# Performance work log

Measured on AMD Instinct MI355X. Metric: run time of the kernel, lower is better.

## Reference

```python
import jax, jax.numpy as jnp
import numpy as np

BN_EPS = 1e-3
SLOPE = 0.1
K = 100
CLUSTER_TEMP = 5.0


def setup_inputs() -> dict:
    key = jax.random.key(0)
    ks = jax.random.split(key, 5)
    N, Cin, Cout = 8192, 1, 64
    d = 49 * Cout  # (28/4)^2 * out_channels
    return {
        "x": jax.random.normal(ks[0], (N, Cin, 28, 28), jnp.float32),
        "conv1_w": jax.random.normal(ks[1], (128, Cin, 5, 5), jnp.float32) * 0.05,
        "conv1_b": jnp.zeros((128,), jnp.float32),
        "bn1_gamma": jnp.ones((128,), jnp.float32),
        "bn1_beta": jnp.zeros((128,), jnp.float32),
        "bn1_mean": jnp.zeros((128,), jnp.float32),
        "bn1_var": jnp.ones((128,), jnp.float32),
        "conv2_w": jax.random.normal(ks[2], (Cout, 128, 5, 5), jnp.float32) * 0.02,
        "conv2_b": jnp.zeros((Cout,), jnp.float32),
        "bn2_gamma": jnp.ones((Cout,), jnp.float32),
        "bn2_beta": jnp.zeros((Cout,), jnp.float32),
        "bn2_mean": jnp.zeros((Cout,), jnp.float32),
        "bn2_var": jnp.ones((Cout,), jnp.float32),
        "init_mu": jax.random.uniform(ks[3], (K, d), jnp.float32),
        "num_iter": 10,
    }


def _conv_bn_lrelu(x, w, b, gamma, beta, mean, var):
    # Conv2d(k=5, s=2, p=2) -> BatchNorm (eval/running stats) -> LeakyReLU(0.1)
    h = jax.lax.conv_general_dilated(
        x, w, window_strides=(2, 2), padding=[(2, 2), (2, 2)],
        dimension_numbers=("NCHW", "OIHW", "NCHW"))
    h = h + b[None, :, None, None]
    inv = gamma * jax.lax.rsqrt(var + BN_EPS)
    h = h * inv[None, :, None, None] + (beta - mean * inv)[None, :, None, None]
    return jnp.where(h >= 0, h, SLOPE * h)


def _cluster(data, mu, num_iter):
    # Row L2-normalize (equivalent to diag(1/||row||) @ data)
    data = data / jnp.linalg.norm(data, axis=1, keepdims=True)  # [n, d]
    for _ in range(num_iter):
        dist = data @ mu.T                                 # [n, K]
        r = jax.nn.softmax(CLUSTER_TEMP * dist, axis=1)    # [n, K]
        cluster_r = r.sum(axis=0)                          # [K]
        cluster_mean = r.T @ data                          # [K, d]
        mu = cluster_mean / cluster_r[:, None]
    dist = data @ mu.T
    r = jax.nn.softmax(CLUSTER_TEMP * dist, axis=1)
    return mu, r, dist


def reference(x, conv1_w, conv1_b, bn1_gamma, bn1_beta, bn1_mean, bn1_var,
              conv2_w, conv2_b, bn2_gamma, bn2_beta, bn2_mean, bn2_var,
              init_mu, num_iter):
    h = _conv_bn_lrelu(x, conv1_w, conv1_b, bn1_gamma, bn1_beta, bn1_mean, bn1_var)
    h = _conv_bn_lrelu(h, conv2_w, conv2_b, bn2_gamma, bn2_beta, bn2_mean, bn2_var)
    embeds = h.reshape(h.shape[0], -1)                     # [N, 49*Cout]
    mu_init, _, _ = _cluster(embeds, init_mu, int(num_iter))
    mu, r, dist = _cluster(embeds, jax.lax.stop_gradient(mu_init), 1)
    return mu, r, dist
```

## Files before the change

kernel.cpp:

```cpp
#include <hip/hip_runtime.h>
#include <hip/hip_bf16.h>
#include <math.h>

#define BN_EPS 1e-3f
#define SLOPE  0.1f
#define TEMP   5.0f
#define DDIM   3136

typedef __attribute__((ext_vector_type(8))) short bf16x8;
typedef __attribute__((ext_vector_type(4))) float f32x4;

static __device__ __forceinline__ short f2b(float f) {
  __hip_bfloat16 h = __float2bfloat16(f);
  return *reinterpret_cast<short*>(&h);
}

#define W2B_OFF   0u
#define W1B_OFF   102400u
#define DB_OFF    204800u
#define DB_SZ     (8192u*3136u/2u)
#define DT_OFF    (DB_OFF + DB_SZ)
#define DT_SZ     (8192u*3136u/2u)
#define MUB_OFF   (DT_OFF + DT_SZ)
#define MUB_SZ    (112u*3136u/2u)
#define MUF_OFF   (MUB_OFF + MUB_SZ)
#define MUF_SZ    (100u*3136u)
#define CMS_OFF   (MUF_OFF + MUF_SZ)
#define CMS_SZ    (16u*3136u*112u/2u)
#define RT_OFF    (CMS_OFF + CMS_SZ)
#define RT_SZ     (112u*8192u/2u)
#define CR_OFF    (RT_OFF + RT_SZ)

__global__ __launch_bounds__(256) void k_w2b(const float* __restrict__ w2,
                                             __hip_bfloat16* __restrict__ w2b) {
  int idx = blockIdx.x * 256 + threadIdx.x;
  if (idx >= 204800) return;
  int ci   = idx & 31;
  int lr   = (idx >> 5) & 15;
  int rest = idx >> 9;
  int kk   = rest % 100;
  int oct  = rest / 100;
  int oc   = oct * 16 + lr;
  int tap  = kk >> 2;
  int c    = ((kk & 3) << 5) + ci;
  w2b[idx] = __float2bfloat16(w2[(oc * 128 + c) * 25 + tap]);
}

__global__ __launch_bounds__(256) void k_w1b(const float* __restrict__ w1,
                                             __hip_bfloat16* __restrict__ w1b) {
  int idx = blockIdx.x * 256 + threadIdx.x;
  if (idx >= 4096) return;
  int k   = idx & 31;
  int lr  = (idx >> 5) & 15;
  int oct = idx >> 9;
  int oc  = oct * 16 + lr;
  float v = (k < 25) ? w1[oc * 25 + k] : 0.f;
  w1b[idx] = __float2bfloat16(v);
}

__global__ __launch_bounds__(256) void k_conv(
    const float* __restrict__ x,
    const __hip_bfloat16* __restrict__ w1bh, const float* __restrict__ b1,
    const float* __restrict__ g1,  const float* __restrict__ be1,
    const float* __restrict__ mn1, const float* __restrict__ vr1,
    const __hip_bfloat16* __restrict__ w2bh, const float* __restrict__ b2,
    const float* __restrict__ g2,  const float* __restrict__ be2,
    const float* __restrict__ mn2, const float* __restrict__ vr2,
    __hip_bfloat16* __restrict__ db) {
  __shared__ float xs[1024];
  __shared__ float bn2s[128];
  __shared__ float bn1a[128], bn1b[128];
  __shared__ float nrm[4];
  __shared__ __align__(16) __hip_bfloat16 h1s[197 * 128];

  const int t    = threadIdx.x;
  const int img  = blockIdx.x;
  const int lane = t & 63;
  const int wv   = t >> 6;
  const int lr   = lane & 15;
  const int kg   = lane >> 4;
  const short* w2b = (const short*)w2bh;
  const short* w1b = (const short*)w1bh;

  for (int i = t; i < 1024; i += 256) xs[i] = 0.f;
  if (t < 64) {
    float a2 = g2[t] * rsqrtf(vr2[t] + BN_EPS);
    bn2s[t]      = a2;
    bn2s[64 + t] = b2[t] * a2 + be2[t] - mn2[t] * a2;
    ((unsigned*)(h1s + 196 * 128))[t] = 0u;
  }
  if (t < 128) {
    float a1 = g1[t] * rsqrtf(vr1[t] + BN_EPS);
    bn1a[t] = a1;
    bn1b[t] = b1[t] * a1 + be1[t] - mn1[t] * a1;
  }
  __syncthreads();
  const float* xi = x + (size_t)img * 784;
  for (int i = t; i < 784; i += 256) {
    int yy = i / 28, xx = i % 28;
    xs[(yy + 2) * 32 + (xx + 2)] = xi[i];
  }
  __syncthreads();

  {
    bf16x8 a0 = *(const bf16x8*)(w1b + (2 * wv) * 512 + lr * 32 + kg * 8);
    bf16x8 a1 = *(const bf16x8*)(w1b + (2 * wv + 1) * 512 + lr * 32 + kg * 8);
    for (int pt = 0; pt < 13; ++pt) {
      const int px  = pt * 16 + lr;
      const int pxc = (px < 196) ? px : 195;
      const int oy  = pxc / 14, ox = pxc - 14 * (pxc / 14);
      const float* xb = xs + (2 * oy) * 32 + 2 * ox;
      short bs[8];
#pragma unroll
      for (int j = 0; j < 8; ++j) {
        int k   = kg * 8 + j;
        int tap = (k < 25) ? k : 0;
        int kh  = tap / 5, kw = tap - 5 * (tap / 5);
        bs[j] = f2b(xb[kh * 32 + kw]);
      }
      bf16x8 b;
#pragma unroll
      for (int j = 0; j < 8; ++j) b[j] = bs[j];
      f32x4 c0 = {0.f, 0.f, 0.f, 0.f}, c1 = {0.f, 0.f, 0.f, 0.f};
      c0 = __builtin_amdgcn_mfma_f32_16x16x32_bf16(a0, b, c0, 0, 0, 0);
      c1 = __builtin_amdgcn_mfma_f32_16x16x32_bf16(a1, b, c1, 0, 0, 0);
      if (px < 196) {
        const int swz = (px & 7) << 4;
        unsigned w0lo, w0hi, w1lo, w1hi;
        {
          float v[4], u[4];
#pragma unroll
          for (int r = 0; r < 4; ++r) {
            int oc = wv * 32 + kg * 4 + r;
            float h = c0[r] * bn1a[oc] + bn1b[oc];
            v[r] = (h >= 0.f) ? h : SLOPE * h;
            int oc2 = oc + 16;
            float h2 = c1[r] * bn1a[oc2] + bn1b[oc2];
            u[r] = (h2 >= 0.f) ? h2 : SLOPE * h2;
          }
          w0lo = (unsigned)(unsigned short)f2b(v[0]) |
                 ((unsigned)(unsigned short)f2b(v[1]) << 16);
          w0hi = (unsigned)(unsigned short)f2b(v[2]) |
                 ((unsigned)(unsigned short)f2b(v[3]) << 16);
          w1lo = (unsigned)(unsigned short)f2b(u[0]) |
                 ((unsigned)(unsigned short)f2b(u[1]) << 16);
          w1hi = (unsigned)(unsigned short)f2b(u[2]) |
                 ((unsigned)(unsigned short)f2b(u[3]) << 16);
        }
        char* base = (char*)h1s + px * 256;
        const int o0 = ((wv * 32 + kg * 4) * 2) ^ swz;
        const int o1 = ((wv * 32 + 16 + kg * 4) * 2) ^ swz;
        *(uint2*)(base + o0) = make_uint2(w0lo, w0hi);
        *(uint2*)(base + o1) = make_uint2(w1lo, w1hi);
      }
    }
  }
  __syncthreads();

  const int woff  = lr * 32 + kg * 8;
  const int kgoff = kg << 4;
  int pxA[4], oyA[4], oxA[4];
#pragma unroll
  for (int pt = 0; pt < 4; ++pt) {
    int p = pt * 16 + lr;
    pxA[pt] = p;
    oyA[pt] = p / 7;
    oxA[pt] = p - 7 * oyA[pt];
  }

  f32x4 acc[4][4];
#pragma unroll
  for (int oct = 0; oct < 4; ++oct)
#pragma unroll
    for (int pt = 0; pt < 4; ++pt) acc[oct][pt] = (f32x4){0.f, 0.f, 0.f, 0.f};

  const int s0 = 25 * wv, s1e = s0 + 25;
  int curtap = -1;
  int rowB[4], rowS[4];

  auto loadk = [&](int kk, bf16x8* areg, bf16x8* breg) {
    int tap = kk >> 2;
    if (tap != curtap) {
      curtap = tap;
      int kh = tap / 5, kw = tap - 5 * (tap / 5);
#pragma unroll
      for (int pt = 0; pt < 4; ++pt) {
        int iy = 2 * oyA[pt] - 2 + kh;
        int ix = 2 * oxA[pt] - 2 + kw;
        bool val = (pxA[pt] < 49) & ((unsigned)iy < 14u) & ((unsigned)ix < 14u);
        int ip = val ? iy * 14 + ix : 196;
        rowB[pt] = ip * 256;
        rowS[pt] = (ip & 7) << 4;
      }
    }
    int c01 = (kk & 3) << 6;
#pragma unroll
    for (int oct = 0; oct < 4; ++oct)
      areg[oct] = *(const bf16x8*)(w2b + ((oct * 100 + kk) << 9) + woff);
#pragma unroll
    for (int pt = 0; pt < 4; ++pt)
      breg[pt] = *(const bf16x8*)((const char*)h1s + rowB[pt] +
                                  ((c01 | kgoff) ^ rowS[pt]));
  };

  bf16x8 a[4], b[4], an[4], bn_[4];
  loadk(s0, a, b);
  for (int kk = s0; kk < s1e; ++kk) {
    if (kk + 1 < s1e) loadk(kk + 1, an, bn_);
#pragma unroll
    for (int oct = 0; oct < 4; ++oct)
#pragma unroll
      for (int pt = 0; pt < 4; ++pt)
        acc[oct][pt] = __builtin_amdgcn_mfma_f32_16x16x32_bf16(a[oct], b[pt],
                                                               acc[oct][pt], 0, 0, 0);
#pragma unroll
    for (int q = 0; q < 4; ++q) { a[q] = an[q]; b[q] = bn_[q]; }
  }
  __syncthreads();

  float* red = (float*)h1s;
  if (wv != 0) {
#pragma unroll
    for (int oct = 0; oct < 4; ++oct)
#pragma unroll
      for (int pt = 0; pt < 4; ++pt)
#pragma unroll
        for (int r = 0; r < 4; ++r)
          red[(wv - 1) * 4096 + ((oct * 4 + pt) * 4 + r) * 64 + lane] =
              acc[oct][pt][r];
  }
  __syncthreads();
  if (wv == 0) {
#pragma unroll
    for (int oct = 0; oct < 4; ++oct)
#pragma unroll
      for (int pt = 0; pt < 4; ++pt)
#pragma unroll
        for (int r = 0; r < 4; ++r) {
          const int i = (oct * 4 + pt) * 4 + r;
          float v = acc[oct][pt][r] + red[i * 64 + lane] +
                    red[4096 + i * 64 + lane] + red[8192 + i * 64 + lane];
          red[i * 64 + lane] = v;
        }
  }
  __syncthreads();

  float outv[16];
  float ss = 0.f;
#pragma unroll
  for (int pt = 0; pt < 4; ++pt) {
#pragma unroll
    for (int r = 0; r < 4; ++r) {
      const int i = ((wv * 4 + pt) * 4 + r);
      float v = red[i * 64 + lane];
      const int oc = wv * 16 + kg * 4 + r;
      v = v * bn2s[oc] + bn2s[64 + oc];
      v = (v >= 0.f) ? v : SLOPE * v;
      outv[pt * 4 + r] = v;
      if (pxA[pt] < 49) ss += v * v;
    }
  }
#pragma unroll
  for (int m = 1; m < 64; m <<= 1) ss += __shfl_xor(ss, m, 64);
  if (lane == 0) nrm[wv] = ss;
  __syncthreads();
  const float invn = rsqrtf(nrm[0] + nrm[1] + nrm[2] + nrm[3]);
  __hip_bfloat16* dro = db + (size_t)img * DDIM;
#pragma unroll
  for (int pt = 0; pt < 4; ++pt) {
    if (pxA[pt] < 49) {
#pragma unroll
      for (int r = 0; r < 4; ++r) {
        const int oc = wv * 16 + kg * 4 + r;
        dro[oc * 49 + pxA[pt]] = __float2bfloat16(outv[pt * 4 + r] * invn);
      }
    }
  }
}

__global__ __launch_bounds__(256) void k_tr(const __hip_bfloat16* __restrict__ dbh,
                                            __hip_bfloat16* __restrict__ dTh) {
  __shared__ short tile[64][72];
  const int t   = threadIdx.x;
  const int i   = t >> 2;
  const int seg = t & 3;
  const size_t img0 = (size_t)blockIdx.x * 64;
  const size_t d0   = (size_t)blockIdx.y * 64;
  const short* src = (const short*)dbh + (img0 + i) * DDIM + d0 + seg * 16;
  bf16x8 v0 = *(const bf16x8*)src;
  bf16x8 v1 = *(const bf16x8*)(src + 8);
  *(bf16x8*)&tile[i][seg * 16]     = v0;
  *(bf16x8*)&tile[i][seg * 16 + 8] = v1;
  __syncthreads();
  short tmp[16];
#pragma unroll
  for (int k = 0; k < 16; ++k) tmp[k] = tile[seg * 16 + k][i];
  short* dst = (short*)dTh + (d0 + i) * 8192 + img0 + seg * 16;
  *(bf16x8*)dst       = *(bf16x8*)tmp;
  *(bf16x8*)(dst + 8) = *((bf16x8*)tmp + 1);
}

__global__ __launch_bounds__(256) void k_muinit(const float* __restrict__ mu0,
                                                __hip_bfloat16* __restrict__ mub) {
  int idx = blockIdx.x * 256 + threadIdx.x;
  if (idx >= 112 * DDIM) return;
  int j = idx / DDIM, d = idx - j * DDIM;
  float v = (j < 100) ? mu0[j * DDIM + d] : 0.f;
  mub[idx] = __float2bfloat16(v);
}

__global__ __launch_bounds__(512) void k_dsm(
    const __hip_bfloat16* __restrict__ data,
    const __hip_bfloat16* __restrict__ mu,
    __hip_bfloat16* __restrict__ rT,
    float* __restrict__ cr,
    float* __restrict__ outr,
    float* __restrict__ outd,
    int final_flag) {
  __shared__ float red[7][64][29];
  const int t    = threadIdx.x;
  const int lane = t & 63;
  const int wv   = t >> 6;
  const int rowbase = blockIdx.x * 16;
  const int s0 = (98 * wv) >> 3;
  const int s1 = (98 * (wv + 1)) >> 3;
  const int lr = lane & 15;
  const int kg = lane >> 4;

  const __hip_bfloat16* arow = data + (size_t)(rowbase + lr) * DDIM + kg * 8;
  const __hip_bfloat16* brow = mu + (size_t)lr * DDIM + kg * 8;

  f32x4 acc[7];
#pragma unroll
  for (int i = 0; i < 7; ++i) acc[i] = (f32x4){0.f, 0.f, 0.f, 0.f};

  bf16x8 a, b[7], an, bn_[7];
  {
    const int k0 = s0 * 32;
    a = *(const bf16x8*)(arow + k0);
#pragma unroll
    for (int tl = 0; tl < 7; ++tl)
      b[tl] = *(const bf16x8*)(brow + (size_t)tl * 16 * DDIM + k0);
  }
  for (int s = s0; s < s1; ++s) {
    if (s + 1 < s1) {
      const int k1 = (s + 1) * 32;
      an = *(const bf16x8*)(arow + k1);
#pragma unroll
      for (int tl = 0; tl < 7; ++tl)
        bn_[tl] = *(const bf16x8*)(brow + (size_t)tl * 16 * DDIM + k1);
    }
#pragma unroll
    for (int tl = 0; tl < 7; ++tl)
      acc[tl] = __builtin_amdgcn_mfma_f32_16x16x32_bf16(a, b[tl], acc[tl], 0, 0, 0);
    a = an;
#pragma unroll
    for (int tl = 0; tl < 7; ++tl) b[tl] = bn_[tl];
  }

  if (wv != 0) {
#pragma unroll
    for (int tl = 0; tl < 7; ++tl)
#pragma unroll
      for (int r = 0; r < 4; ++r) red[wv - 1][lane][tl * 4 + r] = acc[tl][r];
  }
  __syncthreads();
  if (wv != 0) return;

#pragma unroll
  for (int tl = 0; tl < 7; ++tl)
#pragma unroll
    for (int r = 0; r < 4; ++r) {
      float v = acc[tl][r];
#pragma unroll
      for (int bk = 0; bk < 7; ++bk) v += red[bk][lane][tl * 4 + r];
      acc[tl][r] = v;
    }

  if (final_flag) {
#pragma unroll
    for (int tl = 0; tl < 7; ++tl) {
      const int col = tl * 16 + lr;
      if (col < 100) {
#pragma unroll
        for (int r = 0; r < 4; ++r)
          outd[(size_t)(rowbase + kg * 4 + r) * 100 + col] = acc[tl][r];
      }
    }
  }

#pragma unroll
  for (int r = 0; r < 4; ++r) {
    float m = -1e30f;
#pragma unroll
    for (int tl = 0; tl < 7; ++tl) {
      const bool valid = (tl < 6) || (lr < 4);
      m = fmaxf(m, valid ? acc[tl][r] : -1e30f);
    }
    m = fmaxf(m, __shfl_xor(m, 1, 64));
    m = fmaxf(m, __shfl_xor(m, 2, 64));
    m = fmaxf(m, __shfl_xor(m, 4, 64));
    m = fmaxf(m, __shfl_xor(m, 8, 64));
    float s = 0.f;
    float e[7];
#pragma unroll
    for (int tl = 0; tl < 7; ++tl) {
      const bool valid = (tl < 6) || (lr < 4);
      e[tl] = valid ? __expf(TEMP * (acc[tl][r] - m)) : 0.f;
      s += e[tl];
    }
    s += __shfl_xor(s, 1, 64);
    s += __shfl_xor(s, 2, 64);
    s += __shfl_xor(s, 4, 64);
    s += __shfl_xor(s, 8, 64);
    const float inv = 1.f / s;
#pragma unroll
    for (int tl = 0; tl < 7; ++tl) acc[tl][r] = e[tl] * inv;
  }

  if (final_flag) {
#pragma unroll
    for (int tl = 0; tl < 7; ++tl) {
      const int col = tl * 16 + lr;
      if (col < 100) {
#pragma unroll
        for (int r = 0; r < 4; ++r)
          outr[(size_t)(rowbase + kg * 4 + r) * 100 + col] = acc[tl][r];
      }
    }
    return;
  }

#pragma unroll
  for (int tl = 0; tl < 7; ++tl) {
    const int col = tl * 16 + lr;
    if (col < 100) {
#pragma unroll
      for (int r = 0; r < 4; ++r)
        rT[(size_t)col * 8192 + rowbase + kg * 4 + r] = __float2bfloat16(acc[tl][r]);
    }
  }
  float csum[7];
#pragma unroll
  for (int tl = 0; tl < 7; ++tl) {
    float cs = acc[tl][0] + acc[tl][1] + acc[tl][2] + acc[tl][3];
    cs += __shfl_xor(cs, 16, 64);
    cs += __shfl_xor(cs, 32, 64);
    csum[tl] = cs;
  }
  if (lane < 16) {
#pragma unroll
    for (int tl = 0; tl < 7; ++tl) {
      const int col = tl * 16 + lane;
      if (col < 100) atomicAdd(cr + col, csum[tl]);
    }
  }
}

__global__ __launch_bounds__(256) void k_mu(
    const __hip_bfloat16* __restrict__ dataT,
    const __hip_bfloat16* __restrict__ rT,
    __hip_bfloat16* __restrict__ cms) {
  const int t    = threadIdx.x;
  const int lane = t & 63;
  const int wv   = t >> 6;
  const int mbase = blockIdx.x * 64 + wv * 16;
  const int kbase = blockIdx.y * 512;
  const int lr = lane & 15;
  const int kg = lane >> 4;

  const __hip_bfloat16* arow = dataT + (size_t)(mbase + lr) * 8192 + kbase + kg * 8;
  const __hip_bfloat16* brow = rT + (size_t)lr * 8192 + kbase + kg * 8;

  f32x4 acc[7];
#pragma unroll
  for (int i = 0; i < 7; ++i) acc[i] = (f32x4){0.f, 0.f, 0.f, 0.f};

  bf16x8 a, b[7], an, bn_[7];
  a = *(const bf16x8*)(arow);
#pragma unroll
  for (int tl = 0; tl < 7; ++tl)
    b[tl] = *(const bf16x8*)(brow + (size_t)tl * 16 * 8192);
  for (int s = 0; s < 16; ++s) {
    if (s + 1 < 16) {
      const int k1 = (s + 1) * 32;
      an = *(const bf16x8*)(arow + k1);
#pragma unroll
      for (int tl = 0; tl < 7; ++tl)
        bn_[tl] = *(const bf16x8*)(brow + (size_t)tl * 16 * 8192 + k1);
    }
#pragma unroll
    for (int tl = 0; tl < 7; ++tl)
      acc[tl] = __builtin_amdgcn_mfma_f32_16x16x32_bf16(a, b[tl], acc[tl], 0, 0, 0);
    a = an;
#pragma unroll
    for (int tl = 0; tl < 7; ++tl) b[tl] = bn_[tl];
  }

  __hip_bfloat16* dst = cms + (size_t)blockIdx.y * (3136u * 112u);
#pragma unroll
  for (int tl = 0; tl < 7; ++tl) {
    const int col = tl * 16 + lr;
#pragma unroll
    for (int r = 0; r < 4; ++r)
      dst[(size_t)(mbase + kg * 4 + r) * 112 + col] = __float2bfloat16(acc[tl][r]);
  }
}

__global__ __launch_bounds__(256) void k_upd(const __hip_bfloat16* __restrict__ cms,
                                             const float* __restrict__ cr,
                                             float* __restrict__ muf,
                                             __hip_bfloat16* __restrict__ mub) {
  __shared__ float tile[64][113];
  const int t  = threadIdx.x;
  const int d0 = blockIdx.x * 64;
  for (int e = t; e < 64 * 112; e += 256) {
    int dd = e / 112, jj = e - dd * 112;
    const __hip_bfloat16* p = cms + (size_t)(d0 + dd) * 112 + jj;
    float v = 0.f;
#pragma unroll
    for (int s2 = 0; s2 < 16; ++s2)
      v += __bfloat162float(p[(size_t)s2 * (3136u * 112u)]);
    tile[dd][jj] = v;
  }
  __syncthreads();
  for (int e = t; e < 100 * 64; e += 256) {
    int jj = e >> 6, dd = e & 63;
    float v = tile[dd][jj] / cr[jj];
    muf[(size_t)jj * DDIM + d0 + dd] = v;
    mub[(size_t)jj * DDIM + d0 + dd] = __float2bfloat16(v);
  }
}

extern "C" void kernel_launch(void* const* d_in, const int* in_sizes, int n_in,
                              void* d_out, int out_size, void* d_ws, size_t ws_size,
                              hipStream_t stream) {
  const float* x   = (const float*)d_in[0];
  const float* w1  = (const float*)d_in[1];
  const float* b1  = (const float*)d_in[2];
  const float* g1  = (const float*)d_in[3];
  const float* be1 = (const float*)d_in[4];
  const float* mn1 = (const float*)d_in[5];
  const float* vr1 = (const float*)d_in[6];
  const float* w2  = (const float*)d_in[7];
  const float* b2  = (const float*)d_in[8];
  const float* g2  = (const float*)d_in[9];
  const float* be2 = (const float*)d_in[10];
  const float* mn2 = (const float*)d_in[11];
  const float* vr2 = (const float*)d_in[12];
  const float* mu0 = (const float*)d_in[13];

  float* ws = (float*)d_ws;
  __hip_bfloat16* w2b = (__hip_bfloat16*)(ws + W2B_OFF);
  __hip_bfloat16* w1b = (__hip_bfloat16*)(ws + W1B_OFF);
  __hip_bfloat16* db  = (__hip_bfloat16*)(ws + DB_OFF);
  __hip_bfloat16* dT  = (__hip_bfloat16*)(ws + DT_OFF);
  __hip_bfloat16* mub = (__hip_bfloat16*)(ws + MUB_OFF);
  float*          muf = ws + MUF_OFF;
  __hip_bfloat16* cms = (__hip_bfloat16*)(ws + CMS_OFF);
  __hip_bfloat16* rT  = (__hip_bfloat16*)(ws + RT_OFF);
  float*          cr  = ws + CR_OFF;
  float*          out = (float*)d_out;

  k_w2b<<<800, 256, 0, stream>>>(w2, w2b);
  k_w1b<<<16, 256, 0, stream>>>(w1, w1b);
  k_conv<<<8192, 256, 0, stream>>>(x, w1b, b1, g1, be1, mn1, vr1,
                                   w2b, b2, g2, be2, mn2, vr2, db);
  k_tr<<<dim3(128, 49), 256, 0, stream>>>(db, dT);
  k_muinit<<<(112 * DDIM + 255) / 256, 256, 0, stream>>>(mu0, mub);
  hipMemsetAsync(rT + (size_t)100 * 8192, 0, 12 * 8192 * sizeof(__hip_bfloat16),
                 stream);

  for (int it = 0; it < 11; ++it) {
    hipMemsetAsync(cr, 0, 128 * sizeof(float), stream);
    k_dsm<<<512, 512, 0, stream>>>(db, mub, rT, cr, nullptr, nullptr, 0);
    k_mu<<<dim3(49, 16), 256, 0, stream>>>(dT, rT, cms);
    k_upd<<<49, 256, 0, stream>>>(cms, cr, muf, mub);
  }

  k_dsm<<<512, 512, 0, stream>>>(db, mub, rT, cr, out + 313600, out + 1132800, 1);
  hipMemcpyAsync(out, muf, (size_t)MUF_SZ * sizeof(float),
                 hipMemcpyDeviceToDevice, stream);
}
```

Before: 1.850 ms.

## Merge prep kernels, drop memsets and memcpy, register BN params, bf16 input staging

```diff
diff --git a/kernel.cpp b/kernel.cpp
--- a/kernel.cpp
+++ b/kernel.cpp
@@ -17,45 +17,44 @@
 
 #define W2B_OFF   0u
 #define W1B_OFF   102400u
-#define DB_OFF    204800u
+#define DB_OFF    104448u
 #define DB_SZ     (8192u*3136u/2u)
 #define DT_OFF    (DB_OFF + DB_SZ)
 #define DT_SZ     (8192u*3136u/2u)
 #define MUB_OFF   (DT_OFF + DT_SZ)
 #define MUB_SZ    (112u*3136u/2u)
-#define MUF_OFF   (MUB_OFF + MUB_SZ)
-#define MUF_SZ    (100u*3136u)
-#define CMS_OFF   (MUF_OFF + MUF_SZ)
+#define CMS_OFF   (MUB_OFF + MUB_SZ)
 #define CMS_SZ    (16u*3136u*112u/2u)
 #define RT_OFF    (CMS_OFF + CMS_SZ)
 #define RT_SZ     (112u*8192u/2u)
-#define CR_OFF    (RT_OFF + RT_SZ)
-
-__global__ __launch_bounds__(256) void k_w2b(const float* __restrict__ w2,
-                                             __hip_bfloat16* __restrict__ w2b) {
+#define CRB_OFF   (RT_OFF + RT_SZ)
+
+__global__ __launch_bounds__(256) void k_wprep(const float* __restrict__ w2,
+                                               const float* __restrict__ w1,
+                                               __hip_bfloat16* __restrict__ w2b,
+                                               __hip_bfloat16* __restrict__ w1b) {
   int idx = blockIdx.x * 256 + threadIdx.x;
-  if (idx >= 204800) return;
-  int ci   = idx & 31;
-  int lr   = (idx >> 5) & 15;
-  int rest = idx >> 9;
-  int kk   = rest % 100;
-  int oct  = rest / 100;
-  int oc   = oct * 16 + lr;
-  int tap  = kk >> 2;
-  int c    = ((kk & 3) << 5) + ci;
-  w2b[idx] = __float2bfloat16(w2[(oc * 128 + c) * 25 + tap]);
-}
-
-__global__ __launch_bounds__(256) void k_w1b(const float* __restrict__ w1,
-                                             __hip_bfloat16* __restrict__ w1b) {
-  int idx = blockIdx.x * 256 + threadIdx.x;
-  if (idx >= 4096) return;
-  int k   = idx & 31;
-  int lr  = (idx >> 5) & 15;
-  int oct = idx >> 9;
-  int oc  = oct * 16 + lr;
-  float v = (k < 25) ? w1[oc * 25 + k] : 0.f;
-  w1b[idx] = __float2bfloat16(v);
+  if (idx < 204800) {
+    int ci   = idx & 31;
+    int lr   = (idx >> 5) & 15;
+    int rest = idx >> 9;
+    int kk   = rest % 100;
+    int oct  = rest / 100;
+    int oc   = oct * 16 + lr;
+    int tap  = kk >> 2;
+    int c    = ((kk & 3) << 5) + ci;
+    w2b[idx] = __float2bfloat16(w2[(oc * 128 + c) * 25 + tap]);
+  } else {
+    int j = idx - 204800;
+    if (j < 4096) {
+      int k   = j & 31;
+      int lr  = (j >> 5) & 15;
+      int oct = j >> 9;
+      int oc  = oct * 16 + lr;
+      float v = (k < 25) ? w1[oc * 25 + k] : 0.f;
+      w1b[j] = __float2bfloat16(v);
+    }
+  }
 }
 
 __global__ __launch_bounds__(256) void k_conv(
@@ -67,9 +66,7 @@
     const float* __restrict__ g2,  const float* __restrict__ be2,
     const float* __restrict__ mn2, const float* __restrict__ vr2,
     __hip_bfloat16* __restrict__ db) {
-  __shared__ float xs[1024];
-  __shared__ float bn2s[128];
-  __shared__ float bn1a[128], bn1b[128];
+  __shared__ unsigned short xsb[1024];
   __shared__ float nrm[4];
   __shared__ __align__(16) __hip_bfloat16 h1s[197 * 128];
 
@@ -82,23 +79,31 @@
   const short* w2b = (const short*)w2bh;
   const short* w1b = (const short*)w1bh;
 
-  for (int i = t; i < 1024; i += 256) xs[i] = 0.f;
-  if (t < 64) {
-    float a2 = g2[t] * rsqrtf(vr2[t] + BN_EPS);
-    bn2s[t]      = a2;
-    bn2s[64 + t] = b2[t] * a2 + be2[t] - mn2[t] * a2;
-    ((unsigned*)(h1s + 196 * 128))[t] = 0u;
-  }
-  if (t < 128) {
-    float a1 = g1[t] * rsqrtf(vr1[t] + BN_EPS);
-    bn1a[t] = a1;
-    bn1b[t] = b1[t] * a1 + be1[t] - mn1[t] * a1;
-  }
+  float a1v[8], s1v[8];
+#pragma unroll
+  for (int r = 0; r < 4; ++r) {
+    int oc = wv * 32 + kg * 4 + r;
+    float a = g1[oc] * rsqrtf(vr1[oc] + BN_EPS);
+    a1v[r] = a; s1v[r] = b1[oc] * a + be1[oc] - mn1[oc] * a;
+    int oc2 = oc + 16;
+    float a2_ = g1[oc2] * rsqrtf(vr1[oc2] + BN_EPS);
+    a1v[4 + r] = a2_; s1v[4 + r] = b1[oc2] * a2_ + be1[oc2] - mn1[oc2] * a2_;
+  }
+  float a2v[4], s2v[4];
+#pragma unroll
+  for (int r = 0; r < 4; ++r) {
+    int oc = wv * 16 + kg * 4 + r;
+    float a = g2[oc] * rsqrtf(vr2[oc] + BN_EPS);
+    a2v[r] = a; s2v[r] = b2[oc] * a + be2[oc] - mn2[oc] * a;
+  }
+
+  for (int i = t; i < 1024; i += 256) xsb[i] = 0;
+  if (t < 64) ((unsigned*)(h1s + 196 * 128))[t] = 0u;
   __syncthreads();
   const float* xi = x + (size_t)img * 784;
   for (int i = t; i < 784; i += 256) {
     int yy = i / 28, xx = i % 28;
-    xs[(yy + 2) * 32 + (xx + 2)] = xi[i];
+    xsb[(yy + 2) * 32 + (xx + 2)] = (unsigned short)f2b(xi[i]);
   }
   __syncthreads();
 
@@ -109,14 +114,14 @@
       const int px  = pt * 16 + lr;
       const int pxc = (px < 196) ? px : 195;
       const int oy  = pxc / 14, ox = pxc - 14 * (pxc / 14);
-      const float* xb = xs + (2 * oy) * 32 + 2 * ox;
+      const unsigned short* xb = xsb + (2 * oy) * 32 + 2 * ox;
       short bs[8];
 #pragma unroll
       for (int j = 0; j < 8; ++j) {
         int k   = kg * 8 + j;
         int tap = (k < 25) ? k : 0;
         int kh  = tap / 5, kw = tap - 5 * (tap / 5);
-        bs[j] = f2b(xb[kh * 32 + kw]);
+        bs[j] = (short)xb[kh * 32 + kw];
       }
       bf16x8 b;
 #pragma unroll
@@ -125,28 +130,23 @@
       c0 = __builtin_amdgcn_mfma_f32_16x16x32_bf16(a0, b, c0, 0, 0, 0);
       c1 = __builtin_amdgcn_mfma_f32_16x16x32_bf16(a1, b, c1, 0, 0, 0);
       if (px < 196) {
-        const int swz = (px & 7) << 4;
-        unsigned w0lo, w0hi, w1lo, w1hi;
-        {
-          float v[4], u[4];
-#pragma unroll
-          for (int r = 0; r < 4; ++r) {
-            int oc = wv * 32 + kg * 4 + r;
-            float h = c0[r] * bn1a[oc] + bn1b[oc];
-            v[r] = (h >= 0.f) ? h : SLOPE * h;
-            int oc2 = oc + 16;
-            float h2 = c1[r] * bn1a[oc2] + bn1b[oc2];
-            u[r] = (h2 >= 0.f) ? h2 : SLOPE * h2;
-          }
-          w0lo = (unsigned)(unsigned short)f2b(v[0]) |
-                 ((unsigned)(unsigned short)f2b(v[1]) << 16);
-          w0hi = (unsigned)(unsigned short)f2b(v[2]) |
-                 ((unsigned)(unsigned short)f2b(v[3]) << 16);
-          w1lo = (unsigned)(unsigned short)f2b(u[0]) |
-                 ((unsigned)(unsigned short)f2b(u[1]) << 16);
-          w1hi = (unsigned)(unsigned short)f2b(u[2]) |
-                 ((unsigned)(unsigned short)f2b(u[3]) << 16);
+        const int swz = ((px >> 1) & 7) << 4;
+        float v[4], u[4];
+#pragma unroll
+        for (int r = 0; r < 4; ++r) {
+          float h = c0[r] * a1v[r] + s1v[r];
+          v[r] = (h >= 0.f) ? h : SLOPE * h;
+          float h2 = c1[r] * a1v[4 + r] + s1v[4 + r];
+          u[r] = (h2 >= 0.f) ? h2 : SLOPE * h2;
         }
+        unsigned w0lo = (unsigned)(unsigned short)f2b(v[0]) |
+                        ((unsigned)(unsigned short)f2b(v[1]) << 16);
+        unsigned w0hi = (unsigned)(unsigned short)f2b(v[2]) |
+                        ((unsigned)(unsigned short)f2b(v[3]) << 16);
+        unsigned w1lo = (unsigned)(unsigned short)f2b(u[0]) |
+                        ((unsigned)(unsigned short)f2b(u[1]) << 16);
+        unsigned w1hi = (unsigned)(unsigned short)f2b(u[2]) |
+                        ((unsigned)(unsigned short)f2b(u[3]) << 16);
         char* base = (char*)h1s + px * 256;
         const int o0 = ((wv * 32 + kg * 4) * 2) ^ swz;
         const int o1 = ((wv * 32 + 16 + kg * 4) * 2) ^ swz;
@@ -190,7 +190,7 @@
         bool val = (pxA[pt] < 49) & ((unsigned)iy < 14u) & ((unsigned)ix < 14u);
         int ip = val ? iy * 14 + ix : 196;
         rowB[pt] = ip * 256;
-        rowS[pt] = (ip & 7) << 4;
+        rowS[pt] = ((ip >> 1) & 7) << 4;
       }
     }
     int c01 = (kk & 3) << 6;
@@ -253,8 +253,7 @@
     for (int r = 0; r < 4; ++r) {
       const int i = ((wv * 4 + pt) * 4 + r);
       float v = red[i * 64 + lane];
-      const int oc = wv * 16 + kg * 4 + r;
-      v = v * bn2s[oc] + bn2s[64 + oc];
+      v = v * a2v[r] + s2v[r];
       v = (v >= 0.f) ? v : SLOPE * v;
       outv[pt * 4 + r] = v;
       if (pxA[pt] < 49) ss += v * v;
@@ -287,8 +286,8 @@
   const size_t img0 = (size_t)blockIdx.x * 64;
   const size_t d0   = (size_t)blockIdx.y * 64;
   const short* src = (const short*)dbh + (img0 + i) * DDIM + d0 + seg * 16;
-  bf16x8 v0 = *(const bf16x8*)src;
-  bf16x8 v1 = *(const bf16x8*)(src + 8);
+  bf16x8 v0 = __builtin_nontemporal_load((const bf16x8*)src);
+  bf16x8 v1 = __builtin_nontemporal_load((const bf16x8*)(src + 8));
   *(bf16x8*)&tile[i][seg * 16]     = v0;
   *(bf16x8*)&tile[i][seg * 16 + 8] = v1;
   __syncthreads();
@@ -296,17 +295,23 @@
 #pragma unroll
   for (int k = 0; k < 16; ++k) tmp[k] = tile[seg * 16 + k][i];
   short* dst = (short*)dTh + (d0 + i) * 8192 + img0 + seg * 16;
-  *(bf16x8*)dst       = *(bf16x8*)tmp;
-  *(bf16x8*)(dst + 8) = *((bf16x8*)tmp + 1);
+  __builtin_nontemporal_store(*(bf16x8*)tmp, (bf16x8*)dst);
+  __builtin_nontemporal_store(*((bf16x8*)tmp + 1), (bf16x8*)(dst + 8));
 }
 
 __global__ __launch_bounds__(256) void k_muinit(const float* __restrict__ mu0,
-                                                __hip_bfloat16* __restrict__ mub) {
+                                                __hip_bfloat16* __restrict__ mub,
+                                                __hip_bfloat16* __restrict__ rT,
+                                                float* __restrict__ crb) {
   int idx = blockIdx.x * 256 + threadIdx.x;
-  if (idx >= 112 * DDIM) return;
-  int j = idx / DDIM, d = idx - j * DDIM;
-  float v = (j < 100) ? mu0[j * DDIM + d] : 0.f;
-  mub[idx] = __float2bfloat16(v);
+  if (idx < 112 * DDIM) {
+    int j = idx / DDIM, d = idx - j * DDIM;
+    float v = (j < 100) ? mu0[j * DDIM + d] : 0.f;
+    mub[idx] = __float2bfloat16(v);
+  }
+  if (idx < 12 * 8192)
+    rT[(size_t)100 * 8192 + idx] = __float2bfloat16(0.f);
+  if (idx < 12 * 128) crb[idx] = 0.f;
 }
 
 __global__ __launch_bounds__(512) void k_dsm(
@@ -337,7 +342,7 @@
   bf16x8 a, b[7], an, bn_[7];
   {
     const int k0 = s0 * 32;
-    a = *(const bf16x8*)(arow + k0);
+    a = __builtin_nontemporal_load((const bf16x8*)(arow + k0));
 #pragma unroll
     for (int tl = 0; tl < 7; ++tl)
       b[tl] = *(const bf16x8*)(brow + (size_t)tl * 16 * DDIM + k0);
@@ -345,7 +350,7 @@
   for (int s = s0; s < s1; ++s) {
     if (s + 1 < s1) {
       const int k1 = (s + 1) * 32;
-      an = *(const bf16x8*)(arow + k1);
+      an = __builtin_nontemporal_load((const bf16x8*)(arow + k1));
 #pragma unroll
       for (int tl = 0; tl < 7; ++tl)
         bn_[tl] = *(const bf16x8*)(brow + (size_t)tl * 16 * DDIM + k1);
@@ -435,9 +440,12 @@
   for (int tl = 0; tl < 7; ++tl) {
     const int col = tl * 16 + lr;
     if (col < 100) {
-#pragma unroll
-      for (int r = 0; r < 4; ++r)
-        rT[(size_t)col * 8192 + rowbase + kg * 4 + r] = __float2bfloat16(acc[tl][r]);
+      unsigned lo = (unsigned)(unsigned short)f2b(acc[tl][0]) |
+                    ((unsigned)(unsigned short)f2b(acc[tl][1]) << 16);
+      unsigned hi = (unsigned)(unsigned short)f2b(acc[tl][2]) |
+                    ((unsigned)(unsigned short)f2b(acc[tl][3]) << 16);
+      *(uint2*)((short*)rT + (size_t)col * 8192 + rowbase + kg * 4) =
+          make_uint2(lo, hi);
     }
   }
   float csum[7];
@@ -477,14 +485,14 @@
   for (int i = 0; i < 7; ++i) acc[i] = (f32x4){0.f, 0.f, 0.f, 0.f};
 
   bf16x8 a, b[7], an, bn_[7];
-  a = *(const bf16x8*)(arow);
+  a = __builtin_nontemporal_load((const bf16x8*)arow);
 #pragma unroll
   for (int tl = 0; tl < 7; ++tl)
     b[tl] = *(const bf16x8*)(brow + (size_t)tl * 16 * 8192);
   for (int s = 0; s < 16; ++s) {
     if (s + 1 < 16) {
       const int k1 = (s + 1) * 32;
-      an = *(const bf16x8*)(arow + k1);
+      an = __builtin_nontemporal_load((const bf16x8*)(arow + k1));
 #pragma unroll
       for (int tl = 0; tl < 7; ++tl)
         bn_[tl] = *(const bf16x8*)(brow + (size_t)tl * 16 * 8192 + k1);
@@ -511,10 +519,10 @@
                                              const float* __restrict__ cr,
                                              float* __restrict__ muf,
                                              __hip_bfloat16* __restrict__ mub) {
-  __shared__ float tile[64][113];
+  __shared__ float tile[16][113];
   const int t  = threadIdx.x;
-  const int d0 = blockIdx.x * 64;
-  for (int e = t; e < 64 * 112; e += 256) {
+  const int d0 = blockIdx.x * 16;
+  for (int e = t; e < 16 * 112; e += 256) {
     int dd = e / 112, jj = e - dd * 112;
     const __hip_bfloat16* p = cms + (size_t)(d0 + dd) * 112 + jj;
     float v = 0.f;
@@ -524,8 +532,8 @@
     tile[dd][jj] = v;
   }
   __syncthreads();
-  for (int e = t; e < 100 * 64; e += 256) {
-    int jj = e >> 6, dd = e & 63;
+  for (int e = t; e < 100 * 16; e += 256) {
+    int jj = e >> 4, dd = e & 15;
     float v = tile[dd][jj] / cr[jj];
     muf[(size_t)jj * DDIM + d0 + dd] = v;
     mub[(size_t)jj * DDIM + d0 + dd] = __float2bfloat16(v);
@@ -556,29 +564,24 @@
   __hip_bfloat16* db  = (__hip_bfloat16*)(ws + DB_OFF);
   __hip_bfloat16* dT  = (__hip_bfloat16*)(ws + DT_OFF);
   __hip_bfloat16* mub = (__hip_bfloat16*)(ws + MUB_OFF);
-  float*          muf = ws + MUF_OFF;
   __hip_bfloat16* cms = (__hip_bfloat16*)(ws + CMS_OFF);
   __hip_bfloat16* rT  = (__hip_bfloat16*)(ws + RT_OFF);
-  float*          cr  = ws + CR_OFF;
+  float*          crb = ws + CRB_OFF;
   float*          out = (float*)d_out;
 
-  k_w2b<<<800, 256, 0, stream>>>(w2, w2b);
-  k_w1b<<<16, 256, 0, stream>>>(w1, w1b);
+  k_wprep<<<816, 256, 0, stream>>>(w2, w1, w2b, w1b);
   k_conv<<<8192, 256, 0, stream>>>(x, w1b, b1, g1, be1, mn1, vr1,
                                    w2b, b2, g2, be2, mn2, vr2, db);
   k_tr<<<dim3(128, 49), 256, 0, stream>>>(db, dT);
-  k_muinit<<<(112 * DDIM + 255) / 256, 256, 0, stream>>>(mu0, mub);
-  hipMemsetAsync(rT + (size_t)100 * 8192, 0, 12 * 8192 * sizeof(__hip_bfloat16),
-                 stream);
+  k_muinit<<<1372, 256, 0, stream>>>(mu0, mub, rT, crb);
 
   for (int it = 0; it < 11; ++it) {
-    hipMemsetAsync(cr, 0, 128 * sizeof(float), stream);
-    k_dsm<<<512, 512, 0, stream>>>(db, mub, rT, cr, nullptr, nullptr, 0);
+    k_dsm<<<512, 512, 0, stream>>>(db, mub, rT, crb + it * 128,
+                                   nullptr, nullptr, 0);
     k_mu<<<dim3(49, 16), 256, 0, stream>>>(dT, rT, cms);
-    k_upd<<<49, 256, 0, stream>>>(cms, cr, muf, mub);
-  }
-
-  k_dsm<<<512, 512, 0, stream>>>(db, mub, rT, cr, out + 313600, out + 1132800, 1);
-  hipMemcpyAsync(out, muf, (size_t)MUF_SZ * sizeof(float),
-                 hipMemcpyDeviceToDevice, stream);
-}
+    k_upd<<<196, 256, 0, stream>>>(cms, crb + it * 128, out, mub);
+  }
+
+  k_dsm<<<512, 512, 0, stream>>>(db, mub, rT, crb + 11 * 128,
+                                 out + 313600, out + 1132800, 1);
+}
```

Measured after the change: 1.857 ms. Within noise of the previous version (+0.4%).
